# Performance work log

Hardware: AMD Instinct MI355X
Metric: run time of the kernel (lower is better)

The kernel has to match this reference:

```python
import jax, jax.numpy as jnp
import numpy as np

K = 11            # kernel size
D = K * K         # flow input size = 121
HID = 15          # MADE hidden size
NB = 5            # n_blocks
ALPHA = 1e-6      # post_process inverse-logit alpha
EPS = 1e-5        # BatchNorm eps
SCALE = 2         # 1/scale_factor
LOG2PI = float(np.log(2.0 * np.pi))


def _degrees(block):
    # MAF flips input ordering between successive MADE blocks
    d = jnp.arange(D)
    return d if block % 2 == 0 else d[::-1]


def _masks(deg_in):
    # MADE masks: hidden degrees = arange(HID) % (D-1)
    dh = jnp.arange(HID) % (D - 1)
    m1 = (dh[:, None] >= deg_in[None, :]).astype(jnp.float32)   # [HID, D]
    m2 = (deg_in[:, None] > dh[None, :]).astype(jnp.float32)    # [D, HID] (strict for output)
    m2 = jnp.concatenate([m2, m2], axis=0)                      # [2D, HID] (m and loga share mask)
    return m1, m2


def _made_inverse(u, W1, b1, W2, b2, deg):
    m1, m2 = _masks(deg)
    Wm1 = (W1 * m1).T   # [D, HID]
    Wm2 = (W2 * m2).T   # [HID, 2D]

    def net(x):
        h = jax.nn.relu(x @ Wm1 + b1)
        out = h @ Wm2 + b2
        return out[:, :D], out[:, D:]

    def step(x, i):
        m, loga = net(x)
        x = x.at[:, i].set(u[:, i] * jnp.exp(loga[:, i]) + m[:, i])
        return x, None

    x, _ = jax.lax.scan(step, jnp.zeros_like(u), deg)
    # so evaluating on fully-filled x equals the torch loop's last-iteration loga
    _, loga = net(x)
    return x, loga


def _flow_inverse(u, W1, b1, W2, b2, bn_log_gamma, bn_beta, bn_mean, bn_var):
    # FlowSequential.inverse: iterate blocks in reverse, each block = [MADE, BatchNorm]
    x = u
    sum_ldj = jnp.zeros_like(u)
    for b in reversed(range(NB)):
        # BatchNorm inverse (eval mode, running stats)
        var, mean = bn_var[b], bn_mean[b]
        lg, beta = bn_log_gamma[b], bn_beta[b]
        x = (x - beta) * jnp.exp(-lg) * jnp.sqrt(var + EPS) + mean
        sum_ldj = sum_ldj + (0.5 * jnp.log(var + EPS) - lg)[None, :]
        # MADE inverse
        x, loga = _made_inverse(x, W1[b], b1[b], W2[b], b2[b], _degrees(b))
        sum_ldj = sum_ldj + loga
    return x, sum_ldj


def _post_process(x):
    x = (jax.nn.sigmoid(x) - ALPHA) / (1.0 - 2.0 * ALPHA)
    x = x / jnp.sum(x, axis=1, keepdims=True)   # kernel sums to 1
    return x.reshape(x.shape[0], 1, K, K)


def setup_inputs() -> dict:
    key = jax.random.key(0)
    ks = jax.random.split(key, 10)
    s = 0.1
    return {
        "input_tensor": jax.random.normal(ks[0], (1, 3, 4096, 4096), jnp.float32),
        "kernel_code": jax.random.normal(ks[1], (1, D), jnp.float32),
        "W1": jax.random.normal(ks[2], (NB, HID, D), jnp.float32) * s,
        "b1": jax.random.normal(ks[3], (NB, HID), jnp.float32) * s,
        "W2": jax.random.normal(ks[4], (NB, 2 * D, HID), jnp.float32) * s,
        "b2": jax.random.normal(ks[5], (NB, 2 * D), jnp.float32) * s,
        "bn_log_gamma": jax.random.normal(ks[6], (NB, D), jnp.float32) * s,
        "bn_beta": jax.random.normal(ks[7], (NB, D), jnp.float32) * s,
        "bn_mean": jax.random.normal(ks[8], (NB, D), jnp.float32) * s,
        "bn_var": jax.random.uniform(ks[9], (NB, D), jnp.float32) * 0.5 + 0.5,
    }


def reference(input_tensor, kernel_code, W1, b1, W2, b2, bn_log_gamma, bn_beta, bn_mean, bn_var):
    # kp.inverse: flow inverse + log prob under base dist
    x, sum_ldj = _flow_inverse(kernel_code, W1, b1, W2, b2, bn_log_gamma, bn_beta, bn_mean, bn_var)
    base_lp = jnp.sum(-0.5 * kernel_code**2 - 0.5 * LOG2PI, axis=1)
    logprob = base_lp - jnp.sum(sum_ldj, axis=1)   # (unused downstream, kept for fidelity)
    out_k = _post_process(x)                        # [1,1,K,K]
    # grouped conv + stride-2 subsample: conv-with-stride == full conv then [0::2] slice
    w = jnp.broadcast_to(out_k, (3, 1, K, K))
    out_put = jax.lax.conv_general_dilated(
        input_tensor, w, window_strides=(SCALE, SCALE), padding='VALID',
        dimension_numbers=('NCHW', 'OIHW', 'NCHW'), feature_group_count=3)
    return out_put, out_k[0, 0]
```

## Files before the change

kernel.cpp:

```cpp
#include <hip/hip_runtime.h>

#define DD   121
#define NHID 15
#define NBLK 5
#define KS   11
#define IW   4096
#define OW   2043

#define ROR_ADD(v, N)                                                         \
  v += __int_as_float(__builtin_amdgcn_update_dpp(                            \
      0, __float_as_int(v), 0x120 + (N), 0xF, 0xF, true))

__device__ __forceinline__ void stage_weights(
    float* W1d, float* W2d, float* b2d, float* b1d,
    const float* __restrict__ W1, const float* __restrict__ W2,
    const float* __restrict__ b2, const float* __restrict__ b1,
    int blk, int t0, int nt)
{
    const float* W1b = W1 + blk * NHID * DD;
    const float* W2b = W2 + blk * 2 * DD * NHID;
    const float* b2b = b2 + blk * 2 * DD;
    for (int i = t0; i < NHID * DD; i += nt) W1d[i] = W1b[i];
    for (int k = t0; k < DD * NHID; k += nt) {
        const int idx = k / NHID, j = k - idx * NHID;
        W2d[idx*32 + 2*j]     = W2b[idx*NHID + j];
        W2d[idx*32 + 2*j + 1] = W2b[(DD + idx)*NHID + j];
    }
    for (int i = t0; i < DD; i += nt) {
        W2d[i*32 + 30] = 0.f;
        W2d[i*32 + 31] = 0.f;
        b2d[2*i]     = b2b[i];
        b2d[2*i + 1] = b2b[DD + i];
    }
    for (int i = t0; i < NHID; i += nt) b1d[i] = b1[blk*NHID + i];
}

__global__ __launch_bounds__(128) void flow_kernel(
    const float* __restrict__ kc,
    const float* __restrict__ W1, const float* __restrict__ b1,
    const float* __restrict__ W2, const float* __restrict__ b2,
    const float* __restrict__ lg, const float* __restrict__ beta,
    const float* __restrict__ mean, const float* __restrict__ var,
    float* __restrict__ kout)
{
    __shared__ float xs[DD];
    __shared__ float us[DD];
    __shared__ float W1s[2][NHID * DD];
    __shared__ float W2p[2][DD * 32];
    __shared__ float b2p[2][DD * 2];
    __shared__ float b1s[2][16];

    const int tid  = threadIdx.x;
    const int wv   = tid >> 6;
    const int lane = tid & 63;

    stage_weights(W1s[0], W2p[0], b2p[0], b1s[0], W1, W2, b2, b1, NBLK - 1, tid, 128);
    if (tid < DD) xs[tid] = kc[tid];
    __syncthreads();

    for (int b = NBLK - 1; b >= 0; --b) {
        const int buf = (NBLK - 1 - b) & 1;
        if (wv == 1) {
            if (b > 0)
                stage_weights(W1s[buf^1], W2p[buf^1], b2p[buf^1], b1s[buf^1],
                              W1, W2, b2, b1, b - 1, lane, 64);
        } else {
            for (int i = lane; i < DD; i += 64) {
                float s = sqrtf(var[b*DD + i] + 1e-5f);
                us[i] = (xs[i] - beta[b*DD + i]) * __expf(-lg[b*DD + i]) * s + mean[b*DD + i];
            }
            const int evenb = ((b & 1) == 0);
            if (lane < 16) {
                const int j  = lane;
                const int jc = (j < NHID) ? j : (NHID - 1);
                float pre_h = (j < NHID) ? b1s[buf][j] : 0.f;

                auto step = [&](int t, int iS, float2 wpS, float w1S, float uvS, float2 bpS) {
                    float h  = (j < t && j < NHID) ? fmaxf(pre_h, 0.f) : 0.f;
                    float pm = h * wpS.x;
                    float pa = h * wpS.y;
                    ROR_ADD(pm, 1); ROR_ADD(pa, 1);
                    ROR_ADD(pm, 2); ROR_ADD(pa, 2);
                    ROR_ADD(pm, 4); ROR_ADD(pa, 4);
                    ROR_ADD(pm, 8); ROR_ADD(pa, 8);
                    const float xv = fmaf(uvS, __expf(pa + bpS.y), pm + bpS.x);
                    if (j >= t && j < NHID) pre_h = fmaf(xv, w1S, pre_h);
                    if (j == 0) xs[iS] = xv;
                };

                int iA, iB, iC, iD;
                float2 wpA, wpB, wpC, wpD, bpA, bpB, bpC, bpD;
                float  w1A, w1B, w1C, w1D, uvA, uvB, uvC, uvD;

                #define PRELOAD(S, T) { const int tt = (T);                                 \
                    i##S  = evenb ? tt : (DD - 1 - tt);                                     \
                    wp##S = *(const float2*)&W2p[buf][i##S*32 + 2*j];                       \
                    w1##S = W1s[buf][jc*DD + i##S];                                         \
                    uv##S = us[i##S];                                                       \
                    bp##S = *(const float2*)&b2p[buf][2*i##S]; }

                #define QSTEP(S, TCUR, TNEXT) {                                             \
                    int tt = (TNEXT); if (tt > DD - 1) tt = DD - 1;                         \
                    const int ip = evenb ? tt : (DD - 1 - tt);                              \
                    const float2 wpN = *(const float2*)&W2p[buf][ip*32 + 2*j];              \
                    const float  w1N = W1s[buf][jc*DD + ip];                                \
                    const float  uvN = us[ip];                                              \
                    const float2 bpN = *(const float2*)&b2p[buf][2*ip];                     \
                    step((TCUR), i##S, wp##S, w1##S, uv##S, bp##S);                         \
                    i##S = ip; wp##S = wpN; w1##S = w1N; uv##S = uvN; bp##S = bpN; }

                PRELOAD(A, 0) PRELOAD(B, 1) PRELOAD(C, 2) PRELOAD(D, 3)
                #pragma unroll 1
                for (int it = 0; it < 30; ++it) {
                    QSTEP(A, 4*it + 0, 4*it + 4)
                    QSTEP(B, 4*it + 1, 4*it + 5)
                    QSTEP(C, 4*it + 2, 4*it + 6)
                    QSTEP(D, 4*it + 3, 4*it + 7)
                }
                step(DD - 1, iA, wpA, w1A, uvA, bpA);
                #undef PRELOAD
                #undef QSTEP
            }
        }
        __syncthreads();
    }

    if (tid < 64) {
        const float A = 1e-6f;
        float y0, y1 = 0.f;
        {
            float v = xs[tid];
            y0 = (1.f / (1.f + __expf(-v)) - A) / (1.f - 2.f*A);
        }
        if (tid + 64 < DD) {
            float v = xs[tid + 64];
            y1 = (1.f / (1.f + __expf(-v)) - A) / (1.f - 2.f*A);
        }
        float s = y0 + y1;
        #pragma unroll
        for (int off = 32; off >= 1; off >>= 1) s += __shfl_xor(s, off, 64);
        kout[tid] = y0 / s;
        if (tid + 64 < DD) kout[tid + 64] = y1 / s;
    }
}

__global__ __launch_bounds__(256) void conv_kernel(
    const float* __restrict__ in, const float* __restrict__ kf,
    float* __restrict__ out)
{
    const int tx = threadIdx.x;
    int py = blockIdx.x;
    {
        const int N = (OW + 1) / 2;
        const int q = N / 8, r = N % 8;
        const int xcd = py & 7, idx = py >> 3;
        py = (xcd < r) ? xcd * (q + 1) + idx
                       : r * (q + 1) + (xcd - r) * q + idx;
    }
    const int ch  = blockIdx.y;
    const int oy0 = 2 * py;
    const int gy0 = 4 * py;

    const float* __restrict__ inc  = in  + (size_t)ch * IW * IW;
    float*       __restrict__ outc = out + (size_t)ch * OW * OW;
    const int wbase = 16 * tx;

    float acc0[8] = {0.f,0.f,0.f,0.f,0.f,0.f,0.f,0.f};
    float acc1[8] = {0.f,0.f,0.f,0.f,0.f,0.f,0.f,0.f};

    float4 A0, A1, A2, A3, A4, A5, A6;
    float4 B0, B1, B2, B3, B4, B5, B6;

    #define GLOAD(IY, S0, S1, S2, S3, S4, S5, S6) {                           \
        const int gy_ = gy0 + (IY);                                           \
        const float4 z_ = make_float4(0.f, 0.f, 0.f, 0.f);                    \
        S0 = z_; S1 = z_; S2 = z_; S3 = z_; S4 = z_; S5 = z_; S6 = z_;        \
        if (gy_ < IW) {                                                       \
            const float* rp_ = inc + (size_t)gy_ * IW + wbase;                \
            S0 = *(const float4*)(rp_);      S1 = *(const float4*)(rp_ + 4);  \
            S2 = *(const float4*)(rp_ + 8);  S3 = *(const float4*)(rp_ + 12); \
            if (tx < 255) {                                                   \
                S4 = *(const float4*)(rp_ + 16);                              \
                S5 = *(const float4*)(rp_ + 20);                              \
                S6 = *(const float4*)(rp_ + 24);                              \
            }                                                                 \
        } }

    #define COMPUTE(IY, S0, S1, S2, S3, S4, S5, S6) {                         \
        const float wv[28] = {S0.x,S0.y,S0.z,S0.w, S1.x,S1.y,S1.z,S1.w,       \
                              S2.x,S2.y,S2.z,S2.w, S3.x,S3.y,S3.z,S3.w,       \
                              S4.x,S4.y,S4.z,S4.w, S5.x,S5.y,S5.z,S5.w,       \
                              S6.x,S6.y,S6.z,S6.w};                           \
        const int iy_ = (IY);                                                 \
        if (iy_ <= 10) {                                \
            const float* kr_ = kf + iy_ * KS;                                 \
            _Pragma("unroll")                                                 \
            for (int kx = 0; kx < 11; ++kx) {                                 \
                const float kw_ = kr_[kx];                                    \
                _Pragma("unroll")                                             \
                for (int j = 0; j < 8; ++j)                                   \
                    acc0[j] = fmaf(wv[2*j + kx], kw_, acc0[j]);               \
            }                                                                 \
        }                                                                     \
        if (iy_ >= 2) {                             \
            const float* kr_ = kf + (iy_ - 2) * KS;                           \
            _Pragma("unroll")                                                 \
            for (int kx = 0; kx < 11; ++kx) {                                 \
                const float kw_ = kr_[kx];                                    \
                _Pragma("unroll")                                             \
                for (int j = 0; j < 8; ++j)                                   \
                    acc1[j] = fmaf(wv[2*j + kx], kw_, acc1[j]);               \
            }                                                                 \
        } }

    GLOAD(0, A0, A1, A2, A3, A4, A5, A6)
    #pragma unroll 1
    for (int it = 0; it < 6; ++it) {
        const int iy = 2 * it;
        GLOAD(iy + 1, B0, B1, B2, B3, B4, B5, B6)
        COMPUTE(iy, A0, A1, A2, A3, A4, A5, A6)
        GLOAD(iy + 2, A0, A1, A2, A3, A4, A5, A6)
        COMPUTE(iy + 1, B0, B1, B2, B3, B4, B5, B6)
    }
    COMPUTE(12, A0, A1, A2, A3, A4, A5, A6)
    #undef GLOAD
    #undef COMPUTE

    const int ox0 = 8 * tx;
    {
        float* op = outc + (size_t)oy0 * OW + ox0;
        #pragma unroll
        for (int j = 0; j < 8; ++j)
            if (ox0 + j < OW) op[j] = acc0[j];
    }
    if (oy0 + 1 < OW) {
        float* op = outc + (size_t)(oy0 + 1) * OW + ox0;
        #pragma unroll
        for (int j = 0; j < 8; ++j)
            if (ox0 + j < OW) op[j] = acc1[j];
    }
}

extern "C" void kernel_launch(void* const* d_in, const int* in_sizes, int n_in,
                              void* d_out, int out_size, void* d_ws, size_t ws_size,
                              hipStream_t stream)
{
    const float* in   = (const float*)d_in[0];
    const float* kc   = (const float*)d_in[1];
    const float* W1   = (const float*)d_in[2];
    const float* b1   = (const float*)d_in[3];
    const float* W2   = (const float*)d_in[4];
    const float* b2   = (const float*)d_in[5];
    const float* lg   = (const float*)d_in[6];
    const float* beta = (const float*)d_in[7];
    const float* mean = (const float*)d_in[8];
    const float* var  = (const float*)d_in[9];

    float* out  = (float*)d_out;
    float* kout = out + (size_t)3 * OW * OW;

    flow_kernel<<<dim3(1), dim3(128), 0, stream>>>(kc, W1, b1, W2, b2, lg, beta, mean, var, kout);

    dim3 grid((OW + 1) / 2, 3);
    conv_kernel<<<grid, dim3(256), 0, stream>>>(in, kout, out);
}
```

Before: 203.4 us.

## Restructure conv as per-wave vertical strips with rolling accumulator ring

Each wave now handles a 16-output-row vertical strip of 128 columns, streaming input row pairs once and accumulating into a 6-slot rotating ring of output rows, so each input row is loaded once per strip instead of about 13/4 times across overlapping blocks. The grid becomes 16x32x3 with 2 outputs per lane, and the XCD block remapping is dropped. This cuts redundant global and L2 input reads, but each lane does less work per load, loads are clamped at image edges instead of zeroed, and stores are narrow per-lane scalar writes.

```diff
diff --git a/kernel.cpp b/kernel.cpp
--- a/kernel.cpp
+++ b/kernel.cpp
@@ -144,101 +144,114 @@
     }
 }
 
+#define CH 16
+
 __global__ __launch_bounds__(256) void conv_kernel(
     const float* __restrict__ in, const float* __restrict__ kf,
     float* __restrict__ out)
 {
-    const int tx = threadIdx.x;
-    int py = blockIdx.x;
-    {
-        const int N = (OW + 1) / 2;
-        const int q = N / 8, r = N % 8;
-        const int xcd = py & 7, idx = py >> 3;
-        py = (xcd < r) ? xcd * (q + 1) + idx
-                       : r * (q + 1) + (xcd - r) * q + idx;
-    }
-    const int ch  = blockIdx.y;
-    const int oy0 = 2 * py;
-    const int gy0 = 4 * py;
+    const int tid = threadIdx.x;
+    const int wv  = tid >> 6;
+    const int l   = tid & 63;
+    const int bx  = blockIdx.x;
+    const int by  = blockIdx.y;
+    const int ch  = blockIdx.z;
+    const int sy  = by * 4 + wv;
+    const int oy0 = sy * CH;
+    const int gy0 = oy0 * 2;
+    const int ox0 = bx * 128;
+    const int c0  = ox0 + 2 * l;
+    const int Wb  = 2 * ox0 + 4 * l;
 
     const float* __restrict__ inc  = in  + (size_t)ch * IW * IW;
     float*       __restrict__ outc = out + (size_t)ch * OW * OW;
-    const int wbase = 16 * tx;
-
-    float acc0[8] = {0.f,0.f,0.f,0.f,0.f,0.f,0.f,0.f};
-    float acc1[8] = {0.f,0.f,0.f,0.f,0.f,0.f,0.f,0.f};
-
-    float4 A0, A1, A2, A3, A4, A5, A6;
-    float4 B0, B1, B2, B3, B4, B5, B6;
-
-    #define GLOAD(IY, S0, S1, S2, S3, S4, S5, S6) {                           \
-        const int gy_ = gy0 + (IY);                                           \
-        const float4 z_ = make_float4(0.f, 0.f, 0.f, 0.f);                    \
-        S0 = z_; S1 = z_; S2 = z_; S3 = z_; S4 = z_; S5 = z_; S6 = z_;        \
-        if (gy_ < IW) {                                                       \
-            const float* rp_ = inc + (size_t)gy_ * IW + wbase;                \
-            S0 = *(const float4*)(rp_);      S1 = *(const float4*)(rp_ + 4);  \
-            S2 = *(const float4*)(rp_ + 8);  S3 = *(const float4*)(rp_ + 12); \
-            if (tx < 255) {                                                   \
-                S4 = *(const float4*)(rp_ + 16);                              \
-                S5 = *(const float4*)(rp_ + 20);                              \
-                S6 = *(const float4*)(rp_ + 24);                              \
+
+    const int w0 = (Wb      <= 4092) ? Wb      : 4092;
+    const int w1 = (Wb + 4  <= 4092) ? Wb + 4  : 4092;
+    const int w2 = (Wb + 8  <= 4092) ? Wb + 8  : 4092;
+    const int w3 = (Wb + 12 <= 4092) ? Wb + 12 : 4092;
+
+    float2 acc[6] = {};
+
+    float4 Ae0, Ae1, Ae2, Ae3, Ao0, Ao1, Ao2, Ao3;
+    float4 Be0, Be1, Be2, Be3, Bo0, Bo1, Bo2, Bo3;
+
+    #define LDPAIR(T, E0,E1,E2,E3, O0,O1,O2,O3) {                             \
+        int gye = gy0 + 2*(T);     if (gye > IW-1) gye = IW-1;                \
+        int gyo = gy0 + 2*(T) + 1; if (gyo > IW-1) gyo = IW-1;                \
+        const float* re = inc + (size_t)gye * IW;                             \
+        const float* ro = inc + (size_t)gyo * IW;                             \
+        E0 = *(const float4*)(re + w0);  E1 = *(const float4*)(re + w1);      \
+        E2 = *(const float4*)(re + w2);  E3 = *(const float4*)(re + w3);      \
+        O0 = *(const float4*)(ro + w0);  O1 = *(const float4*)(ro + w1);      \
+        O2 = *(const float4*)(ro + w2);  O3 = *(const float4*)(ro + w3); }
+
+    #define PAIRC(U, E0,E1,E2,E3, O0,O1,O2,O3) {                              \
+        const float ev[16] = {E0.x,E0.y,E0.z,E0.w, E1.x,E1.y,E1.z,E1.w,       \
+                              E2.x,E2.y,E2.z,E2.w, E3.x,E3.y,E3.z,E3.w};      \
+        const float ov[16] = {O0.x,O0.y,O0.z,O0.w, O1.x,O1.y,O1.z,O1.w,       \
+                              O2.x,O2.y,O2.z,O2.w, O3.x,O3.y,O3.z,O3.w};      \
+        _Pragma("unroll")                                                     \
+        for (int a = 0; a < 6; ++a) {                  \
+            const int s = ((U) - a + 6) % 6;                                  \
+            const float* kr = kf + (2*a) * KS;                                \
+            _Pragma("unroll")                                                 \
+            for (int kx = 0; kx < 11; ++kx) {                                 \
+                const float w = kr[kx];                                       \
+                acc[s].x = fmaf(ev[kx],     w, acc[s].x);                     \
+                acc[s].y = fmaf(ev[kx + 2], w, acc[s].y);                     \
+            }                                                                 \
+        }                                                                     \
+        _Pragma("unroll")                                                     \
+        for (int a = 0; a < 5; ++a) {                 \
+            const int s = ((U) - a + 6) % 6;                                  \
+            const float* kr = kf + (2*a + 1) * KS;                            \
+            _Pragma("unroll")                                                 \
+            for (int kx = 0; kx < 11; ++kx) {                                 \
+                const float w = kr[kx];                                       \
+                acc[s].x = fmaf(ov[kx],     w, acc[s].x);                     \
+                acc[s].y = fmaf(ov[kx + 2], w, acc[s].y);                     \
             }                                                                 \
         } }
 
-    #define COMPUTE(IY, S0, S1, S2, S3, S4, S5, S6) {                         \
-        const float wv[28] = {S0.x,S0.y,S0.z,S0.w, S1.x,S1.y,S1.z,S1.w,       \
-                              S2.x,S2.y,S2.z,S2.w, S3.x,S3.y,S3.z,S3.w,       \
-                              S4.x,S4.y,S4.z,S4.w, S5.x,S5.y,S5.z,S5.w,       \
-                              S6.x,S6.y,S6.z,S6.w};                           \
-        const int iy_ = (IY);                                                 \
-        if (iy_ <= 10) {                                \
-            const float* kr_ = kf + iy_ * KS;                                 \
-            _Pragma("unroll")                                                 \
-            for (int kx = 0; kx < 11; ++kx) {                                 \
-                const float kw_ = kr_[kx];                                    \
-                _Pragma("unroll")                                             \
-                for (int j = 0; j < 8; ++j)                                   \
-                    acc0[j] = fmaf(wv[2*j + kx], kw_, acc0[j]);               \
+    #define STORE(U, T) {                                                     \
+        const int sc = ((U) + 1) % 6;                                         \
+        if ((T) >= 5) {                                                       \
+            const int oy = oy0 + (T) - 5;                                     \
+            if (oy < OW) {                                                    \
+                float* op = outc + (size_t)oy * OW + c0;                      \
+                if (c0 < OW)     op[0] = acc[sc].x;                           \
+                if (c0 + 1 < OW) op[1] = acc[sc].y;                           \
             }                                                                 \
         }                                                                     \
-        if (iy_ >= 2) {                             \
-            const float* kr_ = kf + (iy_ - 2) * KS;                           \
-            _Pragma("unroll")                                                 \
-            for (int kx = 0; kx < 11; ++kx) {                                 \
-                const float kw_ = kr_[kx];                                    \
-                _Pragma("unroll")                                             \
-                for (int j = 0; j < 8; ++j)                                   \
-                    acc1[j] = fmaf(wv[2*j + kx], kw_, acc1[j]);               \
-            }                                                                 \
-        } }
-
-    GLOAD(0, A0, A1, A2, A3, A4, A5, A6)
+        acc[sc].x = 0.f; acc[sc].y = 0.f; }
+
+    LDPAIR(0, Ae0,Ae1,Ae2,Ae3, Ao0,Ao1,Ao2,Ao3)
+    int t = 0;
     #pragma unroll 1
-    for (int it = 0; it < 6; ++it) {
-        const int iy = 2 * it;
-        GLOAD(iy + 1, B0, B1, B2, B3, B4, B5, B6)
-        COMPUTE(iy, A0, A1, A2, A3, A4, A5, A6)
-        GLOAD(iy + 2, A0, A1, A2, A3, A4, A5, A6)
-        COMPUTE(iy + 1, B0, B1, B2, B3, B4, B5, B6)
-    }
-    COMPUTE(12, A0, A1, A2, A3, A4, A5, A6)
-    #undef GLOAD
-    #undef COMPUTE
-
-    const int ox0 = 8 * tx;
-    {
-        float* op = outc + (size_t)oy0 * OW + ox0;
-        #pragma unroll
-        for (int j = 0; j < 8; ++j)
-            if (ox0 + j < OW) op[j] = acc0[j];
-    }
-    if (oy0 + 1 < OW) {
-        float* op = outc + (size_t)(oy0 + 1) * OW + ox0;
-        #pragma unroll
-        for (int j = 0; j < 8; ++j)
-            if (ox0 + j < OW) op[j] = acc1[j];
-    }
+    for (int g = 0; g < 3; ++g) {
+        LDPAIR(t+1, Be0,Be1,Be2,Be3, Bo0,Bo1,Bo2,Bo3)
+        PAIRC(0, Ae0,Ae1,Ae2,Ae3, Ao0,Ao1,Ao2,Ao3)  STORE(0, t)  ++t;
+        LDPAIR(t+1, Ae0,Ae1,Ae2,Ae3, Ao0,Ao1,Ao2,Ao3)
+        PAIRC(1, Be0,Be1,Be2,Be3, Bo0,Bo1,Bo2,Bo3)  STORE(1, t)  ++t;
+        LDPAIR(t+1, Be0,Be1,Be2,Be3, Bo0,Bo1,Bo2,Bo3)
+        PAIRC(2, Ae0,Ae1,Ae2,Ae3, Ao0,Ao1,Ao2,Ao3)  STORE(2, t)  ++t;
+        LDPAIR(t+1, Ae0,Ae1,Ae2,Ae3, Ao0,Ao1,Ao2,Ao3)
+        PAIRC(3, Be0,Be1,Be2,Be3, Bo0,Bo1,Bo2,Bo3)  STORE(3, t)  ++t;
+        LDPAIR(t+1, Be0,Be1,Be2,Be3, Bo0,Bo1,Bo2,Bo3)
+        PAIRC(4, Ae0,Ae1,Ae2,Ae3, Ao0,Ao1,Ao2,Ao3)  STORE(4, t)  ++t;
+        LDPAIR(t+1, Ae0,Ae1,Ae2,Ae3, Ao0,Ao1,Ao2,Ao3)
+        PAIRC(5, Be0,Be1,Be2,Be3, Bo0,Bo1,Bo2,Bo3)  STORE(5, t)  ++t;
+    }
+    LDPAIR(t+1, Be0,Be1,Be2,Be3, Bo0,Bo1,Bo2,Bo3)
+    PAIRC(0, Ae0,Ae1,Ae2,Ae3, Ao0,Ao1,Ao2,Ao3)  STORE(0, t)  ++t;
+    LDPAIR(t+1, Ae0,Ae1,Ae2,Ae3, Ao0,Ao1,Ao2,Ao3)
+    PAIRC(1, Be0,Be1,Be2,Be3, Bo0,Bo1,Bo2,Bo3)  STORE(1, t)  ++t;
+    PAIRC(2, Ae0,Ae1,Ae2,Ae3, Ao0,Ao1,Ao2,Ao3)  STORE(2, t)
+
+    #undef LDPAIR
+    #undef PAIRC
+    #undef STORE
 }
 
 extern "C" void kernel_launch(void* const* d_in, const int* in_sizes, int n_in,
@@ -261,6 +274,6 @@
 
     flow_kernel<<<dim3(1), dim3(128), 0, stream>>>(kc, W1, b1, W2, b2, lg, beta, mean, var, kout);
 
-    dim3 grid((OW + 1) / 2, 3);
+    dim3 grid(16, 32, 3);
     conv_kernel<<<grid, dim3(256), 0, stream>>>(in, kout, out);
 }
```

New measurement: 189.9 us (median of 2 runs). 6.7% less time.
